# Performance work log

Hardware: AMD Instinct MI355X
Metric: run time of the kernel (lower is better)

## Reference

```python
import jax, jax.numpy as jnp
import numpy as np


def setup_inputs() -> dict:
    key = jax.random.key(0)
    k1, k2 = jax.random.split(key)
    H, W, N = 256, 256, 2000
    # render points live in pixel coordinates of the HxW image
    img_render_points = jax.random.uniform(k1, (N, 2), dtype=jnp.float32) * jnp.float32(W)
    img_ref = jax.random.uniform(k2, (H, W), dtype=jnp.float32)
    return {"img_render_points": img_render_points, "img_ref": img_ref}


def reference(img_render_points, img_ref):
    # prepare_data: render points reshaped to (N, 2); reference image turned
    # into a full coordinate grid of shape (H*W, 2).
    H, W = img_ref.shape
    dt = img_render_points.dtype
    ys, xs = jnp.meshgrid(jnp.arange(H, dtype=dt), jnp.arange(W, dtype=dt), indexing="ij")
    coords = jnp.stack([xs, ys], axis=-1).reshape(-1, 2)  # (M, 2), M = H*W
    pts = img_render_points.reshape(-1, 2)                # (N, 2)

    # pairwise L2 distances via the ||a-b||^2 = ||a||^2 + ||b||^2 - 2 a.b expansion
    # (avoids materializing the (N, M, 2) broadcast diff tensor)
    d2 = (
        jnp.sum(pts * pts, axis=1)[:, None]
        + jnp.sum(coords * coords, axis=1)[None, :]
        - 2.0 * (pts @ coords.T)
    )  # (N, M)
    d = jnp.sqrt(jnp.maximum(d2, 0.0))

    # bidirectional Chamfer: sum of per-render-point min + sum of per-pixel min
    return jnp.sum(jnp.min(d, axis=1)) + jnp.sum(jnp.min(d, axis=0))
```

## Files before the change

### kernel.cpp

```cpp
#include <hip/hip_runtime.h>
#include <math.h>


#define NCHUNK 16
#define SP_CAP 512
#define GRID_W 256

__global__ __launch_bounds__(256) void chamfer_pixel_chunk(
    const float* __restrict__ pts, int N, int chunkLen,
    unsigned int* __restrict__ wsmin, float* __restrict__ out) {
    if (blockIdx.x == 0 && blockIdx.y == 0 && threadIdx.x == 0) out[0] = 0.0f;

    __shared__ float2 sp[SP_CAP];
    const int base = blockIdx.y * chunkLen;
    const int cnt  = min(chunkLen, N - base);
    if (cnt <= 0) return;

    for (int j = threadIdx.x; j < cnt; j += 256)
        sp[j] = ((const float2*)pts)[base + j];
    __syncthreads();

    const int t = threadIdx.x;
    const float c0 = (float)(2 * (t & 127));
    const float c1 = c0 + 1.0f;
    const int rbase = blockIdx.x * 8 + (t >> 7) * 4;
    const float r0 = (float)rbase;
    const float r1 = (float)(rbase + 1);
    const float r2 = (float)(rbase + 2);
    const float r3 = (float)(rbase + 3);

    const float INF = 3.4e38f;
    float m00 = INF, m01 = INF, m10 = INF, m11 = INF;
    float m20 = INF, m21 = INF, m30 = INF, m31 = INF;

#pragma unroll 2
    for (int j = 0; j < cnt; ++j) {
        const float2 p = sp[j];
        const float dx0 = p.x - c0, dx1 = p.x - c1;
        const float dxs0 = dx0 * dx0, dxs1 = dx1 * dx1;
        float dy;
        dy = p.y - r0;
        m00 = fminf(m00, fmaf(dy, dy, dxs0));
        m01 = fminf(m01, fmaf(dy, dy, dxs1));
        dy = p.y - r1;
        m10 = fminf(m10, fmaf(dy, dy, dxs0));
        m11 = fminf(m11, fmaf(dy, dy, dxs1));
        dy = p.y - r2;
        m20 = fminf(m20, fmaf(dy, dy, dxs0));
        m21 = fminf(m21, fmaf(dy, dy, dxs1));
        dy = p.y - r3;
        m30 = fminf(m30, fmaf(dy, dy, dxs0));
        m31 = fminf(m31, fmaf(dy, dy, dxs1));
    }

    const int ci0 = 2 * (t & 127);
    unsigned int* w0 = wsmin + rbase * GRID_W + ci0;
    atomicMin(w0 + 0 * GRID_W + 0, __float_as_uint(m00));
    atomicMin(w0 + 0 * GRID_W + 1, __float_as_uint(m01));
    atomicMin(w0 + 1 * GRID_W + 0, __float_as_uint(m10));
    atomicMin(w0 + 1 * GRID_W + 1, __float_as_uint(m11));
    atomicMin(w0 + 2 * GRID_W + 0, __float_as_uint(m20));
    atomicMin(w0 + 2 * GRID_W + 1, __float_as_uint(m21));
    atomicMin(w0 + 3 * GRID_W + 0, __float_as_uint(m30));
    atomicMin(w0 + 3 * GRID_W + 1, __float_as_uint(m31));
}

__global__ __launch_bounds__(256) void chamfer_reduce(
    const unsigned int* __restrict__ wsmin, const float* __restrict__ pts,
    int N, int H, int W, float* __restrict__ out) {
    __shared__ float red[4];
    const int gid = blockIdx.x * 256 + threadIdx.x;
    float s = 0.0f;

    if (gid * 4 < H * W) {
        uint4 v = ((const uint4*)wsmin)[gid];
        s = sqrtf(__uint_as_float(v.x)) + sqrtf(__uint_as_float(v.y)) +
            sqrtf(__uint_as_float(v.z)) + sqrtf(__uint_as_float(v.w));
    }

    if (blockIdx.x == 0) {
        for (int i = threadIdx.x; i < N; i += 256) {
            float2 p = ((const float2*)pts)[i];
            float nx = fminf(fmaxf(rintf(p.x), 0.0f), (float)(W - 1));
            float ny = fminf(fmaxf(rintf(p.y), 0.0f), (float)(H - 1));
            float dx = p.x - nx, dy = p.y - ny;
            s += sqrtf(fmaf(dx, dx, dy * dy));
        }
    }

    for (int off = 32; off > 0; off >>= 1)
        s += __shfl_down(s, off, 64);
    const int lane = threadIdx.x & 63;
    const int wid  = threadIdx.x >> 6;
    if (lane == 0) red[wid] = s;
    __syncthreads();
    if (threadIdx.x == 0)
        atomicAdd(out, red[0] + red[1] + red[2] + red[3]);
}

extern "C" void kernel_launch(void* const* d_in, const int* in_sizes, int n_in,
                              void* d_out, int out_size, void* d_ws, size_t ws_size,
                              hipStream_t stream) {
    const float* pts = (const float*)d_in[0];
    const int N = in_sizes[0] / 2;
    const int W = GRID_W;
    const int H = in_sizes[1] / W;
    float* out = (float*)d_out;
    unsigned int* wsmin = (unsigned int*)d_ws;

    hipMemsetAsync(d_ws, 0xFF, (size_t)H * W * sizeof(unsigned int), stream);

    const int chunkLen = (N + NCHUNK - 1) / NCHUNK;
    dim3 grid(H / 8, NCHUNK);
    chamfer_pixel_chunk<<<grid, 256, 0, stream>>>(pts, N, chunkLen, wsmin, out);

    const int rblocks = (H * W / 4 + 255) / 256;
    chamfer_reduce<<<rblocks, 256, 0, stream>>>(wsmin, pts, N, H, W, out);
}
```

Before: 71.23 us.

## Replace atomicMin workspace with per-chunk partial minima and chunk-reduce pass

Each pixel-block now writes its partial minima to a dedicated slice of the workspace per point chunk, using plain float2 stores instead of global atomicMin. The reduce kernel then takes the minimum across all chunk slices before the sqrt and sum. This removes the memset launch and the atomic contention. The chunk count is doubled to 32 with a smaller shared buffer, which adds blocks for parallelism but costs 32x more workspace traffic in the reduce pass.

```diff
diff --git a/kernel.cpp b/kernel.cpp
--- a/kernel.cpp
+++ b/kernel.cpp
@@ -2,26 +2,26 @@
 #include <math.h>
 
 
-#define NCHUNK 16
-#define SP_CAP 512
 #define GRID_W 256
+#define NCHUNK 32
+#define SP_CAP 256
 
-__global__ __launch_bounds__(256) void chamfer_pixel_chunk(
-    const float* __restrict__ pts, int N, int chunkLen,
-    unsigned int* __restrict__ wsmin, float* __restrict__ out) {
+__global__ __launch_bounds__(256) void chamfer_pixel_partial(
+    const float* __restrict__ pts, int N, int chunkLen, int M,
+    float* __restrict__ wspart, float* __restrict__ out) {
     if (blockIdx.x == 0 && blockIdx.y == 0 && threadIdx.x == 0) out[0] = 0.0f;
 
     __shared__ float2 sp[SP_CAP];
     const int base = blockIdx.y * chunkLen;
     const int cnt  = min(chunkLen, N - base);
-    if (cnt <= 0) return;
 
     for (int j = threadIdx.x; j < cnt; j += 256)
         sp[j] = ((const float2*)pts)[base + j];
     __syncthreads();
 
     const int t = threadIdx.x;
-    const float c0 = (float)(2 * (t & 127));
+    const int ci0 = 2 * (t & 127);
+    const float c0 = (float)ci0;
     const float c1 = c0 + 1.0f;
     const int rbase = blockIdx.x * 8 + (t >> 7) * 4;
     const float r0 = (float)rbase;
@@ -53,30 +53,31 @@
         m31 = fminf(m31, fmaf(dy, dy, dxs1));
     }
 
-    const int ci0 = 2 * (t & 127);
-    unsigned int* w0 = wsmin + rbase * GRID_W + ci0;
-    atomicMin(w0 + 0 * GRID_W + 0, __float_as_uint(m00));
-    atomicMin(w0 + 0 * GRID_W + 1, __float_as_uint(m01));
-    atomicMin(w0 + 1 * GRID_W + 0, __float_as_uint(m10));
-    atomicMin(w0 + 1 * GRID_W + 1, __float_as_uint(m11));
-    atomicMin(w0 + 2 * GRID_W + 0, __float_as_uint(m20));
-    atomicMin(w0 + 2 * GRID_W + 1, __float_as_uint(m21));
-    atomicMin(w0 + 3 * GRID_W + 0, __float_as_uint(m30));
-    atomicMin(w0 + 3 * GRID_W + 1, __float_as_uint(m31));
+    float2* w = (float2*)(wspart + (size_t)blockIdx.y * M) +
+                (size_t)rbase * (GRID_W / 2) + (ci0 >> 1);
+    const int rs = GRID_W / 2;
+    w[0 * rs] = make_float2(m00, m01);
+    w[1 * rs] = make_float2(m10, m11);
+    w[2 * rs] = make_float2(m20, m21);
+    w[3 * rs] = make_float2(m30, m31);
 }
 
 __global__ __launch_bounds__(256) void chamfer_reduce(
-    const unsigned int* __restrict__ wsmin, const float* __restrict__ pts,
-    int N, int H, int W, float* __restrict__ out) {
+    const float* __restrict__ wspart, const float* __restrict__ pts,
+    int N, int M, int H, int W, float* __restrict__ out) {
     __shared__ float red[4];
     const int gid = blockIdx.x * 256 + threadIdx.x;
-    float s = 0.0f;
 
-    if (gid * 4 < H * W) {
-        uint4 v = ((const uint4*)wsmin)[gid];
-        s = sqrtf(__uint_as_float(v.x)) + sqrtf(__uint_as_float(v.y)) +
-            sqrtf(__uint_as_float(v.z)) + sqrtf(__uint_as_float(v.w));
+    const float INF = 3.4e38f;
+    float m0 = INF, m1 = INF, m2 = INF, m3 = INF;
+#pragma unroll
+    for (int c = 0; c + 4 <= NCHUNK; c += 4) {
+        m0 = fminf(m0, wspart[(size_t)(c + 0) * M + gid]);
+        m1 = fminf(m1, wspart[(size_t)(c + 1) * M + gid]);
+        m2 = fminf(m2, wspart[(size_t)(c + 2) * M + gid]);
+        m3 = fminf(m3, wspart[(size_t)(c + 3) * M + gid]);
     }
+    float s = sqrtf(fminf(fminf(m0, m1), fminf(m2, m3)));
 
     if (blockIdx.x == 0) {
         for (int i = threadIdx.x; i < N; i += 256) {
@@ -105,15 +106,13 @@
     const int N = in_sizes[0] / 2;
     const int W = GRID_W;
     const int H = in_sizes[1] / W;
+    const int M = H * W;
     float* out = (float*)d_out;
-    unsigned int* wsmin = (unsigned int*)d_ws;
-
-    hipMemsetAsync(d_ws, 0xFF, (size_t)H * W * sizeof(unsigned int), stream);
+    float* wspart = (float*)d_ws;
 
     const int chunkLen = (N + NCHUNK - 1) / NCHUNK;
     dim3 grid(H / 8, NCHUNK);
-    chamfer_pixel_chunk<<<grid, 256, 0, stream>>>(pts, N, chunkLen, wsmin, out);
+    chamfer_pixel_partial<<<grid, 256, 0, stream>>>(pts, N, chunkLen, M, wspart, out);
 
-    const int rblocks = (H * W / 4 + 255) / 256;
-    chamfer_reduce<<<rblocks, 256, 0, stream>>>(wsmin, pts, N, H, W, out);
+    chamfer_reduce<<<M / 256, 256, 0, stream>>>(wspart, pts, N, M, H, W, out);
 }
```

New measurement: 70.39 us. No clear change (-1.2%).
